# Performance work log

Measured on AMD Instinct MI355X. Metric: run time of the kernel, lower is better.

## Reference

```python
import jax, jax.numpy as jnp
import numpy as np

N = 100000          # nodes
E = 600000          # edges (avg degree ~6, mesh graph)
C_IN = 6            # input features (xyz + normals)
H = 64              # hidden channels per PointTransformerConv
OUT = 10            # out_channels
NEG_SLOPE = 0.01    # F.leaky_relu default slope
IN_DIMS = [C_IN, C_IN + H, C_IN + 2 * H, C_IN + 3 * H]


def _lin(key, fin, fout):
    return jax.random.normal(key, (fin, fout), jnp.float32) / np.float32(np.sqrt(fin))


def setup_inputs() -> dict:
    key = jax.random.key(0)
    ks = jax.random.split(key, 40)
    inp = {
        "x": jax.random.normal(ks[0], (N, C_IN), jnp.float32),
        "edge_index": jax.random.randint(ks[1], (2, E), 0, N, jnp.int32),
    }
    k = 2
    for l, fin in enumerate(IN_DIMS, start=1):
        inp[f"w{l}_lin"] = _lin(ks[k], fin, H); k += 1   # value projection (bias=False)
        inp[f"w{l}_src"] = _lin(ks[k], fin, H); k += 1   # attention src projection
        inp[f"w{l}_dst"] = _lin(ks[k], fin, H); k += 1   # attention dst projection
        inp[f"w{l}_pos"] = _lin(ks[k], fin, H); k += 1   # positional MLP (Linear)
        inp[f"b{l}_pos"] = jnp.zeros((H,), jnp.float32)
    inp["w_mlp1"] = _lin(ks[k], C_IN + 4 * H, H); k += 1
    inp["b_mlp1"] = jnp.zeros((H,), jnp.float32)
    inp["w_mlp2"] = _lin(ks[k], H, OUT); k += 1
    inp["b_mlp2"] = jnp.zeros((OUT,), jnp.float32)
    return inp


def _ptconv(x, src, dst, w_lin, w_src, w_dst, w_pos, b_pos):
    """PointTransformerConv with x serving as both features and positions.
    message = softmax_i(a_dst[i] - a_src[j] + delta_ij) * (h[j] + delta_ij),
    delta_ij = pos_nn(x_i - x_j); sum-aggregated over incoming edges."""
    h = x @ w_lin                                   # [N,H] values
    a_src = x @ w_src                               # [N,H]
    a_dst = x @ w_dst                               # [N,H]
    delta = (x[dst] - x[src]) @ w_pos + b_pos       # [E,H] pos_nn(pos_i - pos_j)
    alpha = a_dst[dst] - a_src[src] + delta         # [E,H] per-edge, per-channel logits
    # numerically stable segment softmax over edges grouped by destination node
    amax = jax.ops.segment_max(alpha, dst, num_segments=N)      # [N,H]
    e = jnp.exp(alpha - amax[dst])                              # [E,H]
    denom = jax.ops.segment_sum(e, dst, num_segments=N)         # [N,H]
    w = e / (denom[dst] + 1e-16)                                # [E,H]
    return jax.ops.segment_sum(w * (h[src] + delta), dst, num_segments=N)  # [N,H]


def _forward(x, edge_index, ps):
    src, dst = edge_index[0], edge_index[1]
    lrelu = lambda v: jnp.where(v > 0, v, NEG_SLOPE * v)
    x1 = _ptconv(x, src, dst, *ps[0])
    x2 = lrelu(_ptconv(jnp.concatenate([x, x1], 1), src, dst, *ps[1]))
    x3 = lrelu(_ptconv(jnp.concatenate([x, x1, x2], 1), src, dst, *ps[2]))
    x4 = lrelu(_ptconv(jnp.concatenate([x, x1, x2, x3], 1), src, dst, *ps[3]))
    out = jnp.concatenate([x, x1, x2, x3, x4], 1)   # [N, 262]
    w_mlp1, b_mlp1, w_mlp2, b_mlp2 = ps[4]
    out = out @ w_mlp1 + b_mlp1                     # dropout = identity (eval mode)
    return out @ w_mlp2 + b_mlp2                    # [N, OUT]


def reference(x, edge_index,
              w1_lin, w1_src, w1_dst, w1_pos, b1_pos,
              w2_lin, w2_src, w2_dst, w2_pos, b2_pos,
              w3_lin, w3_src, w3_dst, w3_pos, b3_pos,
              w4_lin, w4_src, w4_dst, w4_pos, b4_pos,
              w_mlp1, b_mlp1, w_mlp2, b_mlp2):
    ps = [(w1_lin, w1_src, w1_dst, w1_pos, b1_pos),
          (w2_lin, w2_src, w2_dst, w2_pos, b2_pos),
          (w3_lin, w3_src, w3_dst, w3_pos, b3_pos),
          (w4_lin, w4_src, w4_dst, w4_pos, b4_pos),
          (w_mlp1, b_mlp1, w_mlp2, b_mlp2)]
    return _forward(x, edge_index, ps)
```

## Files before the change

kernel.cpp:

```cpp
#include <hip/hip_runtime.h>
#include <hip/hip_fp16.h>

#define NN 100000
#define EE 600000
#define XSB 288
#define SCAN_B 2048
#define LOG2E 1.44269504f

typedef __attribute__((ext_vector_type(8))) short s16x8;
typedef __attribute__((ext_vector_type(4))) float f32x4;

__device__ inline unsigned short f2b(float f) {
    unsigned u = __float_as_uint(f);
    u += 0x7fffu + ((u >> 16) & 1u);
    return (unsigned short)(u >> 16);
}

__device__ inline void accum4(float* d, float* s, const uint4& r) {
    const unsigned* u = (const unsigned*)&r;
#pragma unroll
    for (int ch = 0; ch < 4; ch++) {
        d[ch] += __uint_as_float(u[ch] << 16);
        s[ch] += __uint_as_float(u[ch] & 0xFFFF0000u);
    }
}

__device__ inline void wconv_elem(int idx, int fin,
                                  const float* wlin, const float* wsrc,
                                  const float* wpos, unsigned short* wt) {
    int ks = idx / 6144;
    int rem = idx - ks * 6144;
    int col = rem >> 5, kk = rem & 31;
    int k = ks * 32 + kk;
    int row = (k < 6) ? k : k - 26;
    float val = 0.f;
    if (k < 6 || (k >= 32 && row < fin)) {
        int m = col >> 6, c = col & 63;
        const float* W = (m == 0) ? wlin : (m == 1) ? wsrc : wpos;
        val = W[row * 64 + c];
    }
    wt[idx] = f2b(val);
}

#define O0 1600000
#define O1 1606144
#define O2 1624576
#define O3 1655296
#define O4 1698304
#define O5 1716736
#define O6 2316736
#define O7 2316800

__global__ __launch_bounds__(256) void k_setup(
    const float* __restrict__ x, const int* __restrict__ ei,
    const float* __restrict__ wl0, const float* __restrict__ ws0, const float* __restrict__ wp0,
    const float* __restrict__ wl1, const float* __restrict__ ws1, const float* __restrict__ wp1,
    const float* __restrict__ wl2, const float* __restrict__ ws2, const float* __restrict__ wp2,
    const float* __restrict__ wl3, const float* __restrict__ ws3, const float* __restrict__ wp3,
    const float* __restrict__ w1,
    unsigned short* __restrict__ xb,
    unsigned short* __restrict__ wt0, unsigned short* __restrict__ wt1,
    unsigned short* __restrict__ wt2, unsigned short* __restrict__ wt3,
    unsigned short* __restrict__ w1t, int* __restrict__ deg,
    unsigned* __restrict__ vg) {
    int i = blockIdx.x * 256 + threadIdx.x;
    if (i < O0) {
        int n = i >> 4, c = (i & 15) * 2;
        unsigned lo = (c < 6)     ? (unsigned)f2b(x[n * 6 + c])     : 0u;
        unsigned hi = (c + 1 < 6) ? (unsigned)f2b(x[n * 6 + c + 1]) : 0u;
        *(unsigned*)&xb[(size_t)n * XSB + c] = lo | (hi << 16);
    } else if (i < O1) {
        wconv_elem(i - O0, 6, wl0, ws0, wp0, wt0);
    } else if (i < O2) {
        wconv_elem(i - O1, 70, wl1, ws1, wp1, wt1);
    } else if (i < O3) {
        wconv_elem(i - O2, 134, wl2, ws2, wp2, wt2);
    } else if (i < O4) {
        wconv_elem(i - O3, 198, wl3, ws3, wp3, wt3);
    } else if (i < O5) {
        int idx = i - O4;
        int col = idx / 288, k = idx - col * 288;
        int row = (k < 6) ? k : k - 26;
        bool valid = (k < 6) || (k >= 32 && row < 262);
        w1t[idx] = f2b(valid ? w1[row * 64 + col] : 0.f);
    } else if (i < O6) {
        atomicAdd(&deg[ei[EE + (i - O5)]], 1);
    } else if (i < O7) {
        vg[(size_t)NN * 64 + (i - O6)] = 0u;
    }
}


__global__ __launch_bounds__(256) void k_scan(
    const int* __restrict__ deg, int* __restrict__ rowptr, int* __restrict__ cursor,
    int* __restrict__ bsum, int* __restrict__ bflag) {
    __shared__ int sh[256];
    __shared__ int soff;
    int b = blockIdx.x, t = threadIdx.x;
    int base = b * SCAN_B + t * 8;
    int vals[8], dv[8];
    int s = 0;
#pragma unroll
    for (int j = 0; j < 8; j++) {
        int i = base + j;
        dv[j] = (i < NN) ? deg[i] : 0;
        s += dv[j];
        vals[j] = s;
    }
    sh[t] = s;
    __syncthreads();
    for (int off = 1; off < 256; off <<= 1) {
        int vv = (t >= off) ? sh[t - off] : 0;
        __syncthreads();
        sh[t] += vv;
        __syncthreads();
    }
    int excl = (t > 0) ? sh[t - 1] : 0;
    if (t == 255) {
        bsum[b] = sh[255];
        __threadfence();
        atomicExch(&bflag[b], 1);
    }
    if (t < 64) {
        int v = 0;
        if (t < b) {
            while (atomicAdd(&bflag[t], 0) == 0) {}
            __threadfence();
            v = bsum[t];
        }
#pragma unroll
        for (int m = 1; m < 64; m <<= 1) v += __shfl_xor(v, m);
        if (t == 0) soff = v;
    }
    __syncthreads();
    int off = soff;
#pragma unroll
    for (int j = 0; j < 8; j++) {
        int i = base + j;
        if (i < NN) {
            int incl = vals[j] + excl + off;
            rowptr[i + 1] = incl;
            cursor[i] = incl - dv[j];
        }
    }
    if (b == 0 && t == 0) rowptr[0] = 0;
}

__global__ void k_scatter(const int* __restrict__ ei, int* __restrict__ cursor,
                          int* __restrict__ csrc) {
    int e = blockIdx.x * 256 + threadIdx.x;
    if (e < EE) {
        int d = ei[EE + e];
        int pos = atomicAdd(&cursor[d], 1);
        csrc[pos] = ei[e];
    }
}


template <int KP>
__global__ __launch_bounds__(256) void k_projm(
    const unsigned short* __restrict__ xb, const unsigned short* __restrict__ wt,
    const float* __restrict__ bpos,
    unsigned* __restrict__ vg, __half* __restrict__ qh) {
    __shared__ short wl[192 * 32];
    const int t = threadIdx.x;
    const int w = t >> 6, l = t & 63;
    const int lo = l & 15, hi = l >> 4;
    const int row_w = blockIdx.x * 128 + w * 32;

    f32x4 acc[2][12];
#pragma unroll
    for (int a = 0; a < 2; a++)
#pragma unroll
        for (int i = 0; i < 12; i++) acc[a][i] = (f32x4)0.f;

    const unsigned short* arow0 = xb + (size_t)(row_w + lo) * XSB;
    const unsigned short* arow1 = xb + (size_t)(row_w + 16 + lo) * XSB;
#pragma unroll
    for (int ks = 0; ks < KP / 32; ks++) {
        __syncthreads();
        {
            const uint4* src = (const uint4*)wt + (size_t)ks * 768;
            uint4* dst = (uint4*)wl;
#pragma unroll
            for (int i = 0; i < 3; i++) {
                int idx = i * 256 + t;
                dst[idx ^ ((idx >> 3) & 7)] = src[idx];
            }
        }
        __syncthreads();
        s16x8 af0 = *(const s16x8*)(arow0 + ks * 32 + hi * 8);
        s16x8 af1 = *(const s16x8*)(arow1 + ks * 32 + hi * 8);
#pragma unroll
        for (int ct = 0; ct < 12; ct++) {
            int ridx = (ct * 16 + lo) * 4 + hi;
            s16x8 bf = *(const s16x8*)&wl[(size_t)(ridx ^ ((ridx >> 3) & 7)) * 8];
            acc[0][ct] = __builtin_amdgcn_mfma_f32_16x16x32_bf16(af0, bf, acc[0][ct], 0, 0, 0);
            acc[1][ct] = __builtin_amdgcn_mfma_f32_16x16x32_bf16(af1, bf, acc[1][ct], 0, 0, 0);
        }
    }

#pragma unroll
    for (int tile = 0; tile < 2; tile++) {
#pragma unroll
        for (int r = 0; r < 4; r++) {
            int node = row_w + tile * 16 + hi * 4 + r;
            if (node < NN) {
#pragma unroll
                for (int j = 0; j < 4; j++) {
                    int c = j * 16 + lo;
                    float h  = acc[tile][0 + j][r];
                    float as = acc[tile][4 + j][r];
                    float p  = acc[tile][8 + j][r];
                    size_t o = (size_t)node * 64 + c;
                    float P = __builtin_amdgcn_exp2f(-(as + p) * LOG2E);
                    vg[o] = (unsigned)f2b(P) | ((unsigned)f2b(P * (h - p)) << 16);
                    qh[o] = __float2half(p + bpos[c]);
                }
            }
        }
    }
}


__global__ __launch_bounds__(256) void k_mlp1f(
    const unsigned short* __restrict__ xb, const unsigned short* __restrict__ w1t,
    const float* __restrict__ b1, const float* __restrict__ w2,
    const float* __restrict__ b2, float* __restrict__ out) {
    __shared__ float w2l[64][10];
    __shared__ float b2l[10];
    __shared__ float b1l[64];
    for (int t = threadIdx.x; t < 714; t += 256) {
        if (t < 640) ((float*)w2l)[t] = w2[t];
        else if (t < 650) b2l[t - 640] = b2[t - 640];
        else b1l[t - 650] = b1[t - 650];
    }
    __syncthreads();

    const int w = threadIdx.x >> 6, l = threadIdx.x & 63;
    const int lo = l & 15, hi = l >> 4;
    const int row_w = blockIdx.x * 256 + w * 64;

    f32x4 acc[4][4];
#pragma unroll
    for (int a = 0; a < 4; a++)
#pragma unroll
        for (int b = 0; b < 4; b++) acc[a][b] = (f32x4)0.f;

#pragma unroll
    for (int ks = 0; ks < 9; ks++) {
        const int k0 = ks * 32 + hi * 8;
        s16x8 bf[4];
#pragma unroll
        for (int ct = 0; ct < 4; ct++)
            bf[ct] = *(const s16x8*)(w1t + (size_t)(ct * 16 + lo) * 288 + k0);
#pragma unroll
        for (int rt = 0; rt < 4; rt++) {
            s16x8 af = *(const s16x8*)(xb + (size_t)(row_w + rt * 16 + lo) * XSB + k0);
#pragma unroll
            for (int ct = 0; ct < 4; ct++)
                acc[rt][ct] = __builtin_amdgcn_mfma_f32_16x16x32_bf16(af, bf[ct], acc[rt][ct], 0, 0, 0);
        }
    }

#pragma unroll
    for (int rt = 0; rt < 4; rt++) {
#pragma unroll
        for (int r = 0; r < 4; r++) {
            int node = row_w + rt * 16 + hi * 4 + r;
            float po[10];
#pragma unroll
            for (int o = 0; o < 10; o++) po[o] = 0.f;
#pragma unroll
            for (int ct = 0; ct < 4; ct++) {
                int c = ct * 16 + lo;
                float hv = acc[rt][ct][r] + b1l[c];
#pragma unroll
                for (int o = 0; o < 10; o++) po[o] = fmaf(hv, w2l[c][o], po[o]);
            }
#pragma unroll
            for (int m = 1; m < 16; m <<= 1)
#pragma unroll
                for (int o = 0; o < 10; o++) po[o] += __shfl_xor(po[o], m);
            if (lo == 0 && node < NN) {
                float* op = out + (size_t)node * 10;
#pragma unroll
                for (int o = 0; o < 5; o++)
                    *(float2*)(op + o * 2) = make_float2(po[o * 2] + b2l[o * 2],
                                                         po[o * 2 + 1] + b2l[o * 2 + 1]);
            }
        }
    }
}


template <int RELU>
__global__ __launch_bounds__(256) void k_edge(
    const uint4* __restrict__ vg,
    const uint2* __restrict__ qh,
    const int* __restrict__ rowptr, const int* __restrict__ csrc,
    unsigned short* __restrict__ xb, int col) {
    int l = threadIdx.x & 63;
    int g = l >> 4, lg = l & 15, gbase = g * 16;
    int node = (blockIdx.x * 4 + (threadIdx.x >> 6)) * 4 + g;
    int b = rowptr[node], e = rowptr[node + 1];
    int deg = e - b;
    int pre = csrc[b + lg];
    uint2 qr = qh[(size_t)node * 16 + lg];
    float d[4] = {0.f, 0.f, 0.f, 0.f};
    float s[4] = {0.f, 0.f, 0.f, 0.f};

    int it = 0;
    int degc = min(deg, 16);
    for (; it < degc; it += 4) {
        int i0 = (it < deg)     ? __shfl(pre, gbase + it)     : NN;
        int i1 = (it + 1 < deg) ? __shfl(pre, gbase + it + 1) : NN;
        int i2 = (it + 2 < deg) ? __shfl(pre, gbase + it + 2) : NN;
        int i3 = (it + 3 < deg) ? __shfl(pre, gbase + it + 3) : NN;
        uint4 r0 = vg[(size_t)i0 * 16 + lg];
        uint4 r1 = vg[(size_t)i1 * 16 + lg];
        uint4 r2 = vg[(size_t)i2 * 16 + lg];
        uint4 r3 = vg[(size_t)i3 * 16 + lg];
        accum4(d, s, r0); accum4(d, s, r1); accum4(d, s, r2); accum4(d, s, r3);
    }
    for (; it < deg; ++it) {
        uint4 r0 = vg[(size_t)csrc[b + it] * 16 + lg];
        accum4(d, s, r0);
    }

    float2 q01 = __half22float2(*(const __half2*)&qr.x);
    float2 q23 = __half22float2(*(const __half2*)&qr.y);
    float qv[4] = {q01.x, q01.y, q23.x, q23.y};
    float o[4];
#pragma unroll
    for (int ch = 0; ch < 4; ch++) {
        float v = (s[ch] + qv[ch] * d[ch]) / (d[ch] + 1e-16f);
        if (RELU) v = (v > 0.f) ? v : 0.01f * v;
        o[ch] = v;
    }
    unsigned p01 = (unsigned)f2b(o[0]) | ((unsigned)f2b(o[1]) << 16);
    unsigned p23 = (unsigned)f2b(o[2]) | ((unsigned)f2b(o[3]) << 16);
    *(uint2*)(xb + (size_t)node * XSB + col + 4 * lg) = make_uint2(p01, p23);
}


extern "C" void kernel_launch(void* const* d_in, const int* in_sizes, int n_in,
                              void* d_out, int out_size, void* d_ws, size_t ws_size,
                              hipStream_t stream) {
    const float* x = (const float*)d_in[0];
    const int* ei = (const int*)d_in[1];
    const float* W[4][4];
    const float* BP[4];
    int base = 2;
    for (int l = 0; l < 4; l++) {
        for (int m = 0; m < 4; m++) W[l][m] = (const float*)d_in[base + m];
        BP[l] = (const float*)d_in[base + 4];
        base += 5;
    }
    const float* w1 = (const float*)d_in[22];
    const float* b1 = (const float*)d_in[23];
    const float* w2 = (const float*)d_in[24];
    const float* b2 = (const float*)d_in[25];

    char* wsp = (char*)d_ws;
    size_t off = 0;
    auto alloc = [&](size_t bytes) {
        void* p = wsp + off;
        off += (bytes + 255) & ~(size_t)255;
        return p;
    };
    unsigned short* xb = (unsigned short*)alloc((size_t)(NN + 256) * XSB * 2);
    unsigned* vg = (unsigned*)alloc((size_t)(NN + 1) * 64 * 4);
    __half* qh = (__half*)alloc((size_t)NN * 64 * 2);
    int* deg = (int*)alloc((size_t)NN * 4);
    int* bflag = (int*)alloc(256 * 4);
    int* bsum = (int*)alloc(256 * 4);
    int* rowptr = (int*)alloc((size_t)(NN + 1) * 4);
    int* cursor = (int*)alloc((size_t)NN * 4);
    int* csrc = (int*)alloc((size_t)(EE + 16) * 4);
    const int KPv[4] = {32, 96, 160, 224};
    unsigned short* wt[4];
    for (int l = 0; l < 4; l++) wt[l] = (unsigned short*)alloc((size_t)192 * KPv[l] * 2);
    unsigned short* w1t = (unsigned short*)alloc((size_t)64 * 288 * 2);

    hipMemsetAsync(deg, 0, 400128 + 1024, stream);
    k_setup<<<(O7 + 255) / 256, 256, 0, stream>>>(
        x, ei,
        W[0][0], W[0][1], W[0][3],
        W[1][0], W[1][1], W[1][3],
        W[2][0], W[2][1], W[2][3],
        W[3][0], W[3][1], W[3][3], w1,
        xb, wt[0], wt[1], wt[2], wt[3], w1t, deg, vg);

    int nb = (NN + SCAN_B - 1) / SCAN_B;
    k_scan<<<nb, 256, 0, stream>>>(deg, rowptr, cursor, bsum, bflag);
    k_scatter<<<(EE + 255) / 256, 256, 0, stream>>>(ei, cursor, csrc);

    const int gProj = (NN + 127) / 128;
    const int gEdge = NN / 16;
    const uint4* vgu = (const uint4*)vg;
    const uint2* qh2 = (const uint2*)qh;

    k_projm<32><<<gProj, 256, 0, stream>>>(xb, wt[0], BP[0], vg, qh);
    k_edge<0><<<gEdge, 256, 0, stream>>>(vgu, qh2, rowptr, csrc, xb, 32);
    k_projm<96><<<gProj, 256, 0, stream>>>(xb, wt[1], BP[1], vg, qh);
    k_edge<1><<<gEdge, 256, 0, stream>>>(vgu, qh2, rowptr, csrc, xb, 96);
    k_projm<160><<<gProj, 256, 0, stream>>>(xb, wt[2], BP[2], vg, qh);
    k_edge<1><<<gEdge, 256, 0, stream>>>(vgu, qh2, rowptr, csrc, xb, 160);
    k_projm<224><<<gProj, 256, 0, stream>>>(xb, wt[3], BP[3], vg, qh);
    k_edge<1><<<gEdge, 256, 0, stream>>>(vgu, qh2, rowptr, csrc, xb, 224);

    k_mlp1f<<<(NN + 255) / 256, 256, 0, stream>>>(xb, w1t, b1, w2, b2, (float*)d_out);
}
```

Before: 293.6 us.

## Replace CSR build with fixed-width ELL adjacency plus overflow list

Destination-grouped adjacency is now built directly in the setup kernel as a 16-slot ELL table per node, with edges beyond 16 appended to a global overflow list. This removes the scan and scatter kernels and their launches and inter-block spin synchronisation. Nodes with degree above 16 linearly scan the entire overflow list on every edge layer, which is cheap for the random degree-6 input but degrades badly on skewed graphs. Neighbour order within a node now depends on atomic ordering.

Result: no change. 289.1 us (-1.6%).

```diff
diff --git a/kernel.cpp b/kernel.cpp
--- a/kernel.cpp
+++ b/kernel.cpp
@@ -4,7 +4,6 @@
 #define NN 100000
 #define EE 600000
 #define XSB 288
-#define SCAN_B 2048
 #define LOG2E 1.44269504f
 
 typedef __attribute__((ext_vector_type(8))) short s16x8;
@@ -62,6 +61,7 @@
     unsigned short* __restrict__ wt0, unsigned short* __restrict__ wt1,
     unsigned short* __restrict__ wt2, unsigned short* __restrict__ wt3,
     unsigned short* __restrict__ w1t, int* __restrict__ deg,
+    int* __restrict__ ell, int* __restrict__ ovfc, int* __restrict__ ovf,
     unsigned* __restrict__ vg) {
     int i = blockIdx.x * 256 + threadIdx.x;
     if (i < O0) {
@@ -84,75 +84,18 @@
         bool valid = (k < 6) || (k >= 32 && row < 262);
         w1t[idx] = f2b(valid ? w1[row * 64 + col] : 0.f);
     } else if (i < O6) {
-        atomicAdd(&deg[ei[EE + (i - O5)]], 1);
+        int e = i - O5;
+        int d = ei[EE + e];
+        int pos = atomicAdd(&deg[d], 1);
+        if (pos < 16) {
+            ell[d * 16 + pos] = ei[e];
+        } else {
+            int k = atomicAdd(ovfc, 1);
+            ovf[2 * k] = d;
+            ovf[2 * k + 1] = ei[e];
+        }
     } else if (i < O7) {
         vg[(size_t)NN * 64 + (i - O6)] = 0u;
-    }
-}
-
-
-__global__ __launch_bounds__(256) void k_scan(
-    const int* __restrict__ deg, int* __restrict__ rowptr, int* __restrict__ cursor,
-    int* __restrict__ bsum, int* __restrict__ bflag) {
-    __shared__ int sh[256];
-    __shared__ int soff;
-    int b = blockIdx.x, t = threadIdx.x;
-    int base = b * SCAN_B + t * 8;
-    int vals[8], dv[8];
-    int s = 0;
-#pragma unroll
-    for (int j = 0; j < 8; j++) {
-        int i = base + j;
-        dv[j] = (i < NN) ? deg[i] : 0;
-        s += dv[j];
-        vals[j] = s;
-    }
-    sh[t] = s;
-    __syncthreads();
-    for (int off = 1; off < 256; off <<= 1) {
-        int vv = (t >= off) ? sh[t - off] : 0;
-        __syncthreads();
-        sh[t] += vv;
-        __syncthreads();
-    }
-    int excl = (t > 0) ? sh[t - 1] : 0;
-    if (t == 255) {
-        bsum[b] = sh[255];
-        __threadfence();
-        atomicExch(&bflag[b], 1);
-    }
-    if (t < 64) {
-        int v = 0;
-        if (t < b) {
-            while (atomicAdd(&bflag[t], 0) == 0) {}
-            __threadfence();
-            v = bsum[t];
-        }
-#pragma unroll
-        for (int m = 1; m < 64; m <<= 1) v += __shfl_xor(v, m);
-        if (t == 0) soff = v;
-    }
-    __syncthreads();
-    int off = soff;
-#pragma unroll
-    for (int j = 0; j < 8; j++) {
-        int i = base + j;
-        if (i < NN) {
-            int incl = vals[j] + excl + off;
-            rowptr[i + 1] = incl;
-            cursor[i] = incl - dv[j];
-        }
-    }
-    if (b == 0 && t == 0) rowptr[0] = 0;
-}
-
-__global__ void k_scatter(const int* __restrict__ ei, int* __restrict__ cursor,
-                          int* __restrict__ csrc) {
-    int e = blockIdx.x * 256 + threadIdx.x;
-    if (e < EE) {
-        int d = ei[EE + e];
-        int pos = atomicAdd(&cursor[d], 1);
-        csrc[pos] = ei[e];
     }
 }
 
@@ -298,34 +241,38 @@
 __global__ __launch_bounds__(256) void k_edge(
     const uint4* __restrict__ vg,
     const uint2* __restrict__ qh,
-    const int* __restrict__ rowptr, const int* __restrict__ csrc,
+    const int* __restrict__ deg, const int* __restrict__ ell,
+    const int* __restrict__ ovfc, const int* __restrict__ ovf,
     unsigned short* __restrict__ xb, int col) {
     int l = threadIdx.x & 63;
     int g = l >> 4, lg = l & 15, gbase = g * 16;
     int node = (blockIdx.x * 4 + (threadIdx.x >> 6)) * 4 + g;
-    int b = rowptr[node], e = rowptr[node + 1];
-    int deg = e - b;
-    int pre = csrc[b + lg];
+    int dg = deg[node];
+    int pre = ell[node * 16 + lg];
     uint2 qr = qh[(size_t)node * 16 + lg];
     float d[4] = {0.f, 0.f, 0.f, 0.f};
     float s[4] = {0.f, 0.f, 0.f, 0.f};
 
-    int it = 0;
-    int degc = min(deg, 16);
-    for (; it < degc; it += 4) {
-        int i0 = (it < deg)     ? __shfl(pre, gbase + it)     : NN;
-        int i1 = (it + 1 < deg) ? __shfl(pre, gbase + it + 1) : NN;
-        int i2 = (it + 2 < deg) ? __shfl(pre, gbase + it + 2) : NN;
-        int i3 = (it + 3 < deg) ? __shfl(pre, gbase + it + 3) : NN;
+    int degc = min(dg, 16);
+    for (int it = 0; it < degc; it += 4) {
+        int i0 = (it < dg)     ? __shfl(pre, gbase + it)     : NN;
+        int i1 = (it + 1 < dg) ? __shfl(pre, gbase + it + 1) : NN;
+        int i2 = (it + 2 < dg) ? __shfl(pre, gbase + it + 2) : NN;
+        int i3 = (it + 3 < dg) ? __shfl(pre, gbase + it + 3) : NN;
         uint4 r0 = vg[(size_t)i0 * 16 + lg];
         uint4 r1 = vg[(size_t)i1 * 16 + lg];
         uint4 r2 = vg[(size_t)i2 * 16 + lg];
         uint4 r3 = vg[(size_t)i3 * 16 + lg];
         accum4(d, s, r0); accum4(d, s, r1); accum4(d, s, r2); accum4(d, s, r3);
     }
-    for (; it < deg; ++it) {
-        uint4 r0 = vg[(size_t)csrc[b + it] * 16 + lg];
-        accum4(d, s, r0);
+    if (dg > 16) {
+        int cnt = ovfc[0];
+        for (int i = 0; i < cnt; i++) {
+            if (ovf[2 * i] == node) {
+                uint4 r0 = vg[(size_t)ovf[2 * i + 1] * 16 + lg];
+                accum4(d, s, r0);
+            }
+        }
     }
 
     float2 q01 = __half22float2(*(const __half2*)&qr.x);
@@ -373,28 +320,22 @@
     unsigned* vg = (unsigned*)alloc((size_t)(NN + 1) * 64 * 4);
     __half* qh = (__half*)alloc((size_t)NN * 64 * 2);
     int* deg = (int*)alloc((size_t)NN * 4);
-    int* bflag = (int*)alloc(256 * 4);
-    int* bsum = (int*)alloc(256 * 4);
-    int* rowptr = (int*)alloc((size_t)(NN + 1) * 4);
-    int* cursor = (int*)alloc((size_t)NN * 4);
-    int* csrc = (int*)alloc((size_t)(EE + 16) * 4);
+    int* ovfc = (int*)alloc(256);
+    int* ell = (int*)alloc((size_t)NN * 16 * 4);
+    int* ovf = (int*)alloc((size_t)2 * EE * 4);
     const int KPv[4] = {32, 96, 160, 224};
     unsigned short* wt[4];
     for (int l = 0; l < 4; l++) wt[l] = (unsigned short*)alloc((size_t)192 * KPv[l] * 2);
     unsigned short* w1t = (unsigned short*)alloc((size_t)64 * 288 * 2);
 
-    hipMemsetAsync(deg, 0, 400128 + 1024, stream);
+    hipMemsetAsync(deg, 0, 400128 + 256, stream);
     k_setup<<<(O7 + 255) / 256, 256, 0, stream>>>(
         x, ei,
         W[0][0], W[0][1], W[0][3],
         W[1][0], W[1][1], W[1][3],
         W[2][0], W[2][1], W[2][3],
         W[3][0], W[3][1], W[3][3], w1,
-        xb, wt[0], wt[1], wt[2], wt[3], w1t, deg, vg);
-
-    int nb = (NN + SCAN_B - 1) / SCAN_B;
-    k_scan<<<nb, 256, 0, stream>>>(deg, rowptr, cursor, bsum, bflag);
-    k_scatter<<<(EE + 255) / 256, 256, 0, stream>>>(ei, cursor, csrc);
+        xb, wt[0], wt[1], wt[2], wt[3], w1t, deg, ell, ovfc, ovf, vg);
 
     const int gProj = (NN + 127) / 128;
     const int gEdge = NN / 16;
@@ -402,13 +343,13 @@
     const uint2* qh2 = (const uint2*)qh;
 
     k_projm<32><<<gProj, 256, 0, stream>>>(xb, wt[0], BP[0], vg, qh);
-    k_edge<0><<<gEdge, 256, 0, stream>>>(vgu, qh2, rowptr, csrc, xb, 32);
+    k_edge<0><<<gEdge, 256, 0, stream>>>(vgu, qh2, deg, ell, ovfc, ovf, xb, 32);
     k_projm<96><<<gProj, 256, 0, stream>>>(xb, wt[1], BP[1], vg, qh);
-    k_edge<1><<<gEdge, 256, 0, stream>>>(vgu, qh2, rowptr, csrc, xb, 96);
+    k_edge<1><<<gEdge, 256, 0, stream>>>(vgu, qh2, deg, ell, ovfc, ovf, xb, 96);
     k_projm<160><<<gProj, 256, 0, stream>>>(xb, wt[2], BP[2], vg, qh);
-    k_edge<1><<<gEdge, 256, 0, stream>>>(vgu, qh2, rowptr, csrc, xb, 160);
+    k_edge<1><<<gEdge, 256, 0, stream>>>(vgu, qh2, deg, ell, ovfc, ovf, xb, 160);
     k_projm<224><<<gProj, 256, 0, stream>>>(xb, wt[3], BP[3], vg, qh);
-    k_edge<1><<<gEdge, 256, 0, stream>>>(vgu, qh2, rowptr, csrc, xb, 224);
+    k_edge<1><<<gEdge, 256, 0, stream>>>(vgu, qh2, deg, ell, ovfc, ovf, xb, 224);
 
     k_mlp1f<<<(NN + 255) / 256, 256, 0, stream>>>(xb, w1t, b1, w2, b2, (float*)d_out);
 }
```
